# Performance work log

Measured on AMD Instinct MI355X. Metric: run time of the kernel, lower is better.

The kernel has to match this reference:

```python
import jax, jax.numpy as jnp
import numpy as np

H, W, DIM, B, K = 28, 28, 384, 64, 1
EPS = 1e-5


def setup_inputs() -> dict:
    key = jax.random.key(0)
    k1, k2, k3 = jax.random.split(key, 3)
    L = 1 + K * H * W
    x = jax.random.normal(k1, (B, L, DIM), dtype=jnp.float32)
    w_reduction = jax.random.normal(k2, (2 * DIM, 4 * DIM), dtype=jnp.float32) * 0.02
    w_convert = jax.random.normal(k3, (2 * DIM, DIM), dtype=jnp.float32) * 0.02
    ln_gamma = jnp.ones((4 * DIM,), dtype=jnp.float32)
    ln_beta = jnp.zeros((4 * DIM,), dtype=jnp.float32)
    return {"x": x, "w_reduction": w_reduction, "w_convert": w_convert,
            "ln_gamma": ln_gamma, "ln_beta": ln_beta}


def reference(x, w_reduction, w_convert, ln_gamma, ln_beta):
    Bb, L, C = x.shape
    k = (L - 1) // (H * W)
    cls_token = x[:, 0:1, :]                      # [B,1,C]
    feat = x[:, 1:, :].reshape(Bb, k, H, W, C)
    x0 = feat[:, :, 0::2, 0::2, :]                # [B,k,H/2,W/2,C]
    x1 = feat[:, :, 1::2, 0::2, :]
    x2 = feat[:, :, 0::2, 1::2, :]
    x3 = feat[:, :, 1::2, 1::2, :]
    m = jnp.concatenate([x0, x1, x2, x3], axis=-1)  # [B,k,H/2,W/2,4C]
    m = m.reshape(Bb, k, -1, 4 * C)
    # LayerNorm over last dim
    mu = jnp.mean(m, axis=-1, keepdims=True)
    var = jnp.mean(jnp.square(m - mu), axis=-1, keepdims=True)
    m = (m - mu) * jax.lax.rsqrt(var + EPS) * ln_gamma + ln_beta
    red = jnp.einsum('bknf,of->bkno', m, w_reduction).reshape(Bb, -1, 2 * C)
    cls_out = jnp.einsum('bic,oc->bio', cls_token, w_convert)  # [B,1,2C]
    return jnp.concatenate([cls_out, red], axis=1)
```

## Files before the change

### kernel.cpp

```cpp
#include <hip/hip_runtime.h>
#include <hip/hip_bf16.h>

#define DIMC 384
#define LL 785
#define FDIM 1536
#define ODIM 768
#define NPATCH 196
#define MROWS 12544
#define BATCH 64

typedef __attribute__((ext_vector_type(8))) short bf16x8;
typedef __attribute__((ext_vector_type(4))) float floatx4;
typedef __attribute__((ext_vector_type(4))) unsigned short ushort4v;

#define WS_WBF_OFF  38535168
#define WS_BIAS_OFF 40894464

__device__ __forceinline__ unsigned short f2bf(float f) {
  union { float f; unsigned int u; } v; v.f = f;
  unsigned int u = v.u + 0x7fffu + ((v.u >> 16) & 1u);
  return (unsigned short)(u >> 16);
}

__device__ __forceinline__ void gload_lds16(const void* g, void* l) {
  __builtin_amdgcn_global_load_lds(
      (const __attribute__((address_space(1))) unsigned int*)g,
      (__attribute__((address_space(3))) unsigned int*)l, 16, 0, 0);
}

__global__ __launch_bounds__(256) void prep_kernel(
    const float* __restrict__ x, const float* __restrict__ wred,
    const float* __restrict__ wconv, const float* __restrict__ gamma,
    const float* __restrict__ beta, unsigned short* __restrict__ anorm,
    unsigned short* __restrict__ wbf, float* __restrict__ bias,
    float* __restrict__ out) {
  const int blk = blockIdx.x;
  const int t = threadIdx.x;
  const int wv = t >> 6;
  const int lane = t & 63;

  if (blk < 1568) {
    const int w = blk * 4 + wv;
    const int lane4 = lane * 4;
    float4 v[2][6];
    unsigned int base0[2];
#pragma unroll
    for (int rr = 0; rr < 2; ++rr) {
      int m = w * 2 + rr;
      int b = m / NPATCH;
      int n = m - b * NPATCH;
      int i = n / 14;
      int j = n - i * 14;
      base0[rr] = ((unsigned)b * LL + 1 + (unsigned)(i * 2) * 28 + (unsigned)(j * 2)) * DIMC;
    }
#pragma unroll
    for (int rr = 0; rr < 2; ++rr) {
#pragma unroll
      for (int c = 0; c < 3; ++c) {
        v[rr][c]     = *reinterpret_cast<const float4*>(x + base0[rr] + lane4 + c * 256);
        v[rr][3 + c] = *reinterpret_cast<const float4*>(x + base0[rr] + 28 * DIMC + lane4 + c * 256);
      }
    }
    float s[2] = {0.f, 0.f}, s2[2] = {0.f, 0.f};
#pragma unroll
    for (int rr = 0; rr < 2; ++rr)
#pragma unroll
      for (int c = 0; c < 6; ++c) {
        float4 q = v[rr][c];
        s[rr]  += q.x + q.y + q.z + q.w;
        s2[rr] += q.x * q.x + q.y * q.y + q.z * q.z + q.w * q.w;
      }
#pragma unroll
    for (int o = 1; o < 64; o <<= 1) {
      s[0]  += __shfl_xor(s[0], o);
      s[1]  += __shfl_xor(s[1], o);
      s2[0] += __shfl_xor(s2[0], o);
      s2[1] += __shfl_xor(s2[1], o);
    }
#pragma unroll
    for (int rr = 0; rr < 2; ++rr) {
      int m = w * 2 + rr;
      float mu = s[rr] * (1.f / FDIM);
      float var = s2[rr] * (1.f / FDIM) - mu * mu;
      float rs = rsqrtf(var + 1e-5f);
      float nmu = -mu * rs;
      unsigned short* arow = anorm + (size_t)m * FDIM;
#pragma unroll
      for (int c = 0; c < 6; ++c) {
        int fl = lane4 + (c % 3) * 256;
        int f = fl + ((fl >= 384) ? 384 : 0) + ((c >= 3) ? 384 : 0);
        float4 q = v[rr][c];
        union { ushort4v u4; __hip_bfloat162 h[2]; } u;
        u.h[0] = __float22bfloat162_rn(make_float2(q.x * rs + nmu, q.y * rs + nmu));
        u.h[1] = __float22bfloat162_rn(make_float2(q.z * rs + nmu, q.w * rs + nmu));
        *reinterpret_cast<ushort4v*>(arow + f) = u.u4;
      }
    }
  } else if (blk < 2720) {
    int idx4 = (blk - 1568) * 256 + t;
    int e0 = idx4 * 4;
    int f = e0 % FDIM;
    float4 wq = *reinterpret_cast<const float4*>(wred + e0);
    float4 g = *reinterpret_cast<const float4*>(gamma + f);
    ushort4v u;
    u.x = f2bf(wq.x * g.x); u.y = f2bf(wq.y * g.y);
    u.z = f2bf(wq.z * g.z); u.w = f2bf(wq.w * g.w);
    *reinterpret_cast<ushort4v*>(wbf + e0) = u;
  } else if (blk < 2912) {
    int o = (blk - 2720) * 4 + wv;
    const float* wr = wred + (size_t)o * FDIM;
    float s = 0.f;
#pragma unroll
    for (int c = 0; c < 6; ++c) {
      int f = lane * 4 + c * 256;
      float4 wq = *reinterpret_cast<const float4*>(wr + f);
      float4 be = *reinterpret_cast<const float4*>(beta + f);
      s += wq.x * be.x + wq.y * be.y + wq.z * be.z + wq.w * be.w;
    }
#pragma unroll
    for (int o2 = 32; o2 > 0; o2 >>= 1) s += __shfl_down(s, o2);
    if (lane == 0) bias[o] = s;
  } else {
    __shared__ float xs[DIMC];
    int idx = blk - 2912;
    int b = idx / 3;
    int ch = idx - b * 3;
    for (int c = t; c < DIMC; c += 256) xs[c] = x[(size_t)b * LL * DIMC + c];
    __syncthreads();
    int o = ch * 256 + t;
    const float* wr = wconv + (size_t)o * DIMC;
    float acc = 0.f;
#pragma unroll 4
    for (int c = 0; c < DIMC; c += 4) {
      float4 wq = *reinterpret_cast<const float4*>(wr + c);
      acc += wq.x * xs[c] + wq.y * xs[c + 1] + wq.z * xs[c + 2] + wq.w * xs[c + 3];
    }
    out[(size_t)b * 197 * ODIM + o] = acc;
  }
}

__global__ __launch_bounds__(256) void gemm_kernel(
    const unsigned short* __restrict__ anorm,
    const unsigned short* __restrict__ wbf,
    const float* __restrict__ bias, float* __restrict__ out) {
  __shared__ unsigned short As[128 * 64];
  __shared__ unsigned short Bs[128 * 64];

  const int t = threadIdx.x;
  int id = blockIdx.x;
  int rb, cb;
  if (id < 576) {
    int g = id / 48;
    int rem = id - g * 48;
    rb = g * 8 + (rem & 7);
    cb = rem >> 3;
  } else {
    int r = id - 576;
    rb = 96 + (r & 1);
    cb = r >> 1;
  }
  const int mBase = rb * 128;
  const int nBase = cb * 128;

  const unsigned short* agp[4];
  const unsigned short* bgp[4];
  unsigned int ldsoff[4];
#pragma unroll
  for (int p = 0; p < 4; ++p) {
    int s = p * 256 + t;
    int r = s >> 3;
    int cs = (s & 7) ^ (r & 7);
    agp[p] = anorm + (size_t)(mBase + r) * FDIM + cs * 8;
    bgp[p] = wbf + (size_t)(nBase + r) * FDIM + cs * 8;
    ldsoff[p] = (unsigned)s * 8;
  }

  const int wv = t >> 6;
  const int lane = t & 63;
  const int ln15 = lane & 15;
  const int quad = lane >> 4;
  const int wm = wv >> 1;
  const int wn = wv & 1;

  unsigned int aoff[4][2], boff[4][2];
#pragma unroll
  for (int mt = 0; mt < 4; ++mt) {
#pragma unroll
    for (int h = 0; h < 2; ++h) {
      int rA = wm * 64 + mt * 16 + ln15;
      aoff[mt][h] = (unsigned)(rA * 64 + (((h * 4 + quad) ^ (rA & 7)) * 8));
      int rB = wn * 64 + mt * 16 + ln15;
      boff[mt][h] = (unsigned)(rB * 64 + (((h * 4 + quad) ^ (rB & 7)) * 8));
    }
  }

  floatx4 acc[4][4];
#pragma unroll
  for (int mt = 0; mt < 4; ++mt)
#pragma unroll
    for (int nt = 0; nt < 4; ++nt)
      acc[mt][nt] = floatx4{0.f, 0.f, 0.f, 0.f};

  for (int kt = 0; kt < FDIM / 64; ++kt) {
    if (kt) __syncthreads();
#pragma unroll
    for (int p = 0; p < 4; ++p) {
      gload_lds16(agp[p], &As[ldsoff[p]]);
      gload_lds16(bgp[p], &Bs[ldsoff[p]]);
      agp[p] += 64;
      bgp[p] += 64;
    }
    __syncthreads();

#pragma unroll
    for (int h = 0; h < 2; ++h) {
      bf16x8 af[4], bfr[4];
#pragma unroll
      for (int mt = 0; mt < 4; ++mt)
        af[mt] = *reinterpret_cast<const bf16x8*>(&As[aoff[mt][h]]);
#pragma unroll
      for (int nt = 0; nt < 4; ++nt)
        bfr[nt] = *reinterpret_cast<const bf16x8*>(&Bs[boff[nt][h]]);
#pragma unroll
      for (int mt = 0; mt < 4; ++mt)
#pragma unroll
        for (int nt = 0; nt < 4; ++nt)
          acc[mt][nt] = __builtin_amdgcn_mfma_f32_16x16x32_bf16(
              af[mt], bfr[nt], acc[mt][nt], 0, 0, 0);
    }
  }

  float bs[4];
#pragma unroll
  for (int nt = 0; nt < 4; ++nt)
    bs[nt] = bias[nBase + wn * 64 + nt * 16 + ln15];
#pragma unroll
  for (int mt = 0; mt < 4; ++mt) {
#pragma unroll
    for (int r = 0; r < 4; ++r) {
      int m = mBase + wm * 64 + mt * 16 + quad * 4 + r;
      int b = m / NPATCH;
      int n = m - b * NPATCH;
      float* orow = out + ((size_t)b * 197 + 1 + n) * ODIM + nBase + wn * 64;
#pragma unroll
      for (int nt = 0; nt < 4; ++nt)
        orow[nt * 16 + ln15] = acc[mt][nt][r] + bs[nt];
    }
  }
}

extern "C" void kernel_launch(void* const* d_in, const int* in_sizes, int n_in,
                              void* d_out, int out_size, void* d_ws, size_t ws_size,
                              hipStream_t stream) {
  const float* x     = (const float*)d_in[0];
  const float* wred  = (const float*)d_in[1];
  const float* wconv = (const float*)d_in[2];
  const float* gamma = (const float*)d_in[3];
  const float* beta  = (const float*)d_in[4];
  float* out = (float*)d_out;

  unsigned short* anorm = (unsigned short*)d_ws;
  unsigned short* wbf   = (unsigned short*)((char*)d_ws + WS_WBF_OFF);
  float* bias           = (float*)((char*)d_ws + WS_BIAS_OFF);

  prep_kernel<<<dim3(3104), 256, 0, stream>>>(x, wred, wconv, gamma, beta,
                                              anorm, wbf, bias, out);
  gemm_kernel<<<dim3(588), 256, 0, stream>>>(anorm, wbf, bias, out);
}
```

Baseline: 211.8 us.

## Split LayerNorm prep into stats pass and normalize-write pass

The LayerNorm preprocessing is split into two kernels. The first computes per-row mean and rstd with one wave per row and stores them to a workspace buffer. The second rereads x and writes the normalized bf16 rows, using one wave per half-row. The aim is more parallelism and fewer registers per wave, at the cost of reading x twice and adding one kernel launch.

```diff
diff --git a/kernel.cpp b/kernel.cpp
--- a/kernel.cpp
+++ b/kernel.cpp
@@ -13,8 +13,9 @@
 typedef __attribute__((ext_vector_type(4))) float floatx4;
 typedef __attribute__((ext_vector_type(4))) unsigned short ushort4v;
 
-#define WS_WBF_OFF  38535168
-#define WS_BIAS_OFF 40894464
+#define WS_WBF_OFF   38535168
+#define WS_BIAS_OFF  40894464
+#define WS_STATS_OFF 40897536
 
 __device__ __forceinline__ unsigned short f2bf(float f) {
   union { float f; unsigned int u; } v; v.f = f;
@@ -28,76 +29,50 @@
       (__attribute__((address_space(3))) unsigned int*)l, 16, 0, 0);
 }
 
-__global__ __launch_bounds__(256) void prep_kernel(
+__global__ __launch_bounds__(256) void k1_kernel(
     const float* __restrict__ x, const float* __restrict__ wred,
     const float* __restrict__ wconv, const float* __restrict__ gamma,
-    const float* __restrict__ beta, unsigned short* __restrict__ anorm,
-    unsigned short* __restrict__ wbf, float* __restrict__ bias,
+    const float* __restrict__ beta, unsigned short* __restrict__ wbf,
+    float* __restrict__ bias, float* __restrict__ stats,
     float* __restrict__ out) {
   const int blk = blockIdx.x;
   const int t = threadIdx.x;
   const int wv = t >> 6;
   const int lane = t & 63;
 
-  if (blk < 1568) {
-    const int w = blk * 4 + wv;
+  if (blk < 3136) {
+    const int m = blk * 4 + wv;
+    int b = m / NPATCH;
+    int n = m - b * NPATCH;
+    int i = n / 14;
+    int j = n - i * 14;
+    const unsigned base =
+        ((unsigned)b * LL + 1 + (unsigned)(i * 2) * 28 + (unsigned)(j * 2)) * DIMC;
     const int lane4 = lane * 4;
-    float4 v[2][6];
-    unsigned int base0[2];
-#pragma unroll
-    for (int rr = 0; rr < 2; ++rr) {
-      int m = w * 2 + rr;
-      int b = m / NPATCH;
-      int n = m - b * NPATCH;
-      int i = n / 14;
-      int j = n - i * 14;
-      base0[rr] = ((unsigned)b * LL + 1 + (unsigned)(i * 2) * 28 + (unsigned)(j * 2)) * DIMC;
-    }
-#pragma unroll
-    for (int rr = 0; rr < 2; ++rr) {
+    float s = 0.f, s2 = 0.f;
+#pragma unroll
+    for (int h = 0; h < 2; ++h) {
+      const unsigned rb = base + (unsigned)h * 28 * DIMC;
 #pragma unroll
       for (int c = 0; c < 3; ++c) {
-        v[rr][c]     = *reinterpret_cast<const float4*>(x + base0[rr] + lane4 + c * 256);
-        v[rr][3 + c] = *reinterpret_cast<const float4*>(x + base0[rr] + 28 * DIMC + lane4 + c * 256);
+        float4 q = *reinterpret_cast<const float4*>(x + rb + lane4 + c * 256);
+        s  += q.x + q.y + q.z + q.w;
+        s2 += q.x * q.x + q.y * q.y + q.z * q.z + q.w * q.w;
       }
     }
-    float s[2] = {0.f, 0.f}, s2[2] = {0.f, 0.f};
-#pragma unroll
-    for (int rr = 0; rr < 2; ++rr)
-#pragma unroll
-      for (int c = 0; c < 6; ++c) {
-        float4 q = v[rr][c];
-        s[rr]  += q.x + q.y + q.z + q.w;
-        s2[rr] += q.x * q.x + q.y * q.y + q.z * q.z + q.w * q.w;
-      }
 #pragma unroll
     for (int o = 1; o < 64; o <<= 1) {
-      s[0]  += __shfl_xor(s[0], o);
-      s[1]  += __shfl_xor(s[1], o);
-      s2[0] += __shfl_xor(s2[0], o);
-      s2[1] += __shfl_xor(s2[1], o);
-    }
-#pragma unroll
-    for (int rr = 0; rr < 2; ++rr) {
-      int m = w * 2 + rr;
-      float mu = s[rr] * (1.f / FDIM);
-      float var = s2[rr] * (1.f / FDIM) - mu * mu;
-      float rs = rsqrtf(var + 1e-5f);
-      float nmu = -mu * rs;
-      unsigned short* arow = anorm + (size_t)m * FDIM;
-#pragma unroll
-      for (int c = 0; c < 6; ++c) {
-        int fl = lane4 + (c % 3) * 256;
-        int f = fl + ((fl >= 384) ? 384 : 0) + ((c >= 3) ? 384 : 0);
-        float4 q = v[rr][c];
-        union { ushort4v u4; __hip_bfloat162 h[2]; } u;
-        u.h[0] = __float22bfloat162_rn(make_float2(q.x * rs + nmu, q.y * rs + nmu));
-        u.h[1] = __float22bfloat162_rn(make_float2(q.z * rs + nmu, q.w * rs + nmu));
-        *reinterpret_cast<ushort4v*>(arow + f) = u.u4;
-      }
-    }
-  } else if (blk < 2720) {
-    int idx4 = (blk - 1568) * 256 + t;
+      s  += __shfl_xor(s, o);
+      s2 += __shfl_xor(s2, o);
+    }
+    if (lane == 0) {
+      float mu = s * (1.f / FDIM);
+      float var = s2 * (1.f / FDIM) - mu * mu;
+      stats[2 * m]     = mu;
+      stats[2 * m + 1] = rsqrtf(var + 1e-5f);
+    }
+  } else if (blk < 4288) {
+    int idx4 = (blk - 3136) * 256 + t;
     int e0 = idx4 * 4;
     int f = e0 % FDIM;
     float4 wq = *reinterpret_cast<const float4*>(wred + e0);
@@ -106,8 +81,8 @@
     u.x = f2bf(wq.x * g.x); u.y = f2bf(wq.y * g.y);
     u.z = f2bf(wq.z * g.z); u.w = f2bf(wq.w * g.w);
     *reinterpret_cast<ushort4v*>(wbf + e0) = u;
-  } else if (blk < 2912) {
-    int o = (blk - 2720) * 4 + wv;
+  } else if (blk < 4480) {
+    int o = (blk - 4288) * 4 + wv;
     const float* wr = wred + (size_t)o * FDIM;
     float s = 0.f;
 #pragma unroll
@@ -122,7 +97,7 @@
     if (lane == 0) bias[o] = s;
   } else {
     __shared__ float xs[DIMC];
-    int idx = blk - 2912;
+    int idx = blk - 4480;
     int b = idx / 3;
     int ch = idx - b * 3;
     for (int c = t; c < DIMC; c += 256) xs[c] = x[(size_t)b * LL * DIMC + c];
@@ -136,6 +111,43 @@
       acc += wq.x * xs[c] + wq.y * xs[c + 1] + wq.z * xs[c + 2] + wq.w * xs[c + 3];
     }
     out[(size_t)b * 197 * ODIM + o] = acc;
+  }
+}
+
+__global__ __launch_bounds__(256) void k2_kernel(
+    const float* __restrict__ x, const float* __restrict__ stats,
+    unsigned short* __restrict__ anorm) {
+  const int t = threadIdx.x;
+  const int gw = blockIdx.x * 4 + (t >> 6);
+  const int lane = t & 63;
+  const int m = gw >> 1;
+  const int h = gw & 1;
+  int b = m / NPATCH;
+  int n = m - b * NPATCH;
+  int i = n / 14;
+  int j = n - i * 14;
+  const unsigned base =
+      ((unsigned)b * LL + 1 + (unsigned)(i * 2 + h) * 28 + (unsigned)(j * 2)) * DIMC;
+  const int lane4 = lane * 4;
+
+  float4 v[3];
+#pragma unroll
+  for (int c = 0; c < 3; ++c)
+    v[c] = *reinterpret_cast<const float4*>(x + base + lane4 + c * 256);
+
+  float mu = stats[2 * m];
+  float rs = stats[2 * m + 1];
+  float nmu = -mu * rs;
+
+  unsigned short* arow = anorm + (size_t)m * FDIM + h * 384;
+#pragma unroll
+  for (int c = 0; c < 3; ++c) {
+    int fl = lane4 + c * 256;
+    int f = fl + ((fl >= 384) ? 384 : 0);
+    union { ushort4v u4; __hip_bfloat162 h2[2]; } u;
+    u.h2[0] = __float22bfloat162_rn(make_float2(v[c].x * rs + nmu, v[c].y * rs + nmu));
+    u.h2[1] = __float22bfloat162_rn(make_float2(v[c].z * rs + nmu, v[c].w * rs + nmu));
+    *reinterpret_cast<ushort4v*>(arow + f) = u.u4;
   }
 }
 
@@ -262,8 +274,10 @@
   unsigned short* anorm = (unsigned short*)d_ws;
   unsigned short* wbf   = (unsigned short*)((char*)d_ws + WS_WBF_OFF);
   float* bias           = (float*)((char*)d_ws + WS_BIAS_OFF);
-
-  prep_kernel<<<dim3(3104), 256, 0, stream>>>(x, wred, wconv, gamma, beta,
-                                              anorm, wbf, bias, out);
+  float* stats          = (float*)((char*)d_ws + WS_STATS_OFF);
+
+  k1_kernel<<<dim3(4672), 256, 0, stream>>>(x, wred, wconv, gamma, beta,
+                                            wbf, bias, stats, out);
+  k2_kernel<<<dim3(6272), 256, 0, stream>>>(x, stats, anorm);
   gemm_kernel<<<dim3(588), 256, 0, stream>>>(anorm, wbf, bias, out);
 }
```

After: 226.8 us. +7.1%, slower.
